# Optimization experiments

Measured on AMD Instinct MI355X. Metric: run time of the kernel, lower is better.

Reference implementation:

```python
import jax, jax.numpy as jnp
import numpy as np

B, N, D, S, ITERS, EPS = 32, 4096, 512, 8, 3, 1e-8


def layer_norm(x, g, b, eps=1e-5):
    mu = jnp.mean(x, axis=-1, keepdims=True)
    var = jnp.var(x, axis=-1, keepdims=True)
    return (x - mu) * jax.lax.rsqrt(var + eps) * g + b


def setup_inputs() -> dict:
    key = jax.random.key(0)
    ks = jax.random.split(key, 12)
    sc = 1.0 / np.sqrt(D)
    return {
        "inputs": jax.random.normal(ks[0], (B, N, D), jnp.float32),
        "noise": jax.random.normal(ks[1], (B, S, D), jnp.float32),
        "slots_mu": jax.random.normal(ks[2], (1, S, D), jnp.float32),
        "slots_sigma": jnp.ones((1, S, D), jnp.float32),
        "ln_in_g": jnp.ones((D,), jnp.float32), "ln_in_b": jnp.zeros((D,), jnp.float32),
        "ln_s_g": jnp.ones((D,), jnp.float32), "ln_s_b": jnp.zeros((D,), jnp.float32),
        "wq": jax.random.normal(ks[3], (D, D), jnp.float32) * sc,
        "wk": jax.random.normal(ks[4], (D, D), jnp.float32) * sc,
        "wv": jax.random.normal(ks[5], (D, D), jnp.float32) * sc,
        "w_ih": jax.random.normal(ks[6], (3 * D, D), jnp.float32) * sc,
        "w_hh": jax.random.normal(ks[7], (3 * D, D), jnp.float32) * sc,
        "b_ih": jnp.zeros((3 * D,), jnp.float32),
        "b_hh": jnp.zeros((3 * D,), jnp.float32),
        "ln_m_g": jnp.ones((D,), jnp.float32), "ln_m_b": jnp.zeros((D,), jnp.float32),
        "w1": jax.random.normal(ks[8], (D, D), jnp.float32) * sc,
        "b1": jnp.zeros((D,), jnp.float32),
        "w2": jax.random.normal(ks[9], (D, D), jnp.float32) * sc,
        "b2": jnp.zeros((D,), jnp.float32),
    }


def reference(inputs, noise, slots_mu, slots_sigma, ln_in_g, ln_in_b, ln_s_g, ln_s_b,
              wq, wk, wv, w_ih, w_hh, b_ih, b_hh, ln_m_g, ln_m_b, w1, b1, w2, b2):
    # slot init: mu + sigma * N(0,1)
    slots = slots_mu + slots_sigma * noise          # (B,S,D)
    x = layer_norm(inputs, ln_in_g, ln_in_b)        # (B,N,D)
    k = jnp.einsum('bnd,ed->bne', x, wk)            # (B,N,D)
    v = jnp.einsum('bnd,ed->bne', x, wv)            # (B,N,D)
    for _ in range(ITERS):
        slots_prev = slots
        sn = layer_norm(slots, ln_s_g, ln_s_b)
        q = jnp.einsum('bsd,ed->bse', sn, wq)       # (B,S,D)
        logits = jnp.einsum('bnd,bsd->bns', k, q)   # (B,N,S)
        attn = jax.nn.softmax(logits, axis=-1) + EPS  # softmax over slots
        attn = attn / jnp.sum(attn, axis=-1, keepdims=True)
        attn_t = jnp.swapaxes(attn, -1, -2)         # (B,S,N)
        updates = jnp.einsum('bsn,bnd->bsd', attn_t, v)
        # GRUCell(input=updates, hidden=slots_prev)
        gi = jnp.einsum('bsd,ed->bse', updates, w_ih) + b_ih
        gh = jnp.einsum('bsd,ed->bse', slots_prev, w_hh) + b_hh
        gi_r, gi_z, gi_n = jnp.split(gi, 3, axis=-1)
        gh_r, gh_z, gh_n = jnp.split(gh, 3, axis=-1)
        r = jax.nn.sigmoid(gi_r + gh_r)
        z = jax.nn.sigmoid(gi_z + gh_z)
        n = jnp.tanh(gi_n + r * gh_n)
        slots = (1.0 - z) * n + z * slots_prev
        # residual MLP
        h = layer_norm(slots, ln_m_g, ln_m_b)
        h = jax.nn.relu(jnp.einsum('bsd,ed->bse', h, w1) + b1)
        slots = slots + jnp.einsum('bsd,ed->bse', h, w2) + b2
    return slots
```

## Files before the change

### kernel.cpp

```cpp
#include <hip/hip_runtime.h>

#define B_ 32
#define N_ 4096
#define D_ 512
#define S_ 8
#define ITERS_ 3

__device__ __forceinline__ float sigmoid_f(float x) {
    return 1.0f / (1.0f + __expf(-x));
}
__device__ __forceinline__ float tanh_f(float x) {
    float e = __expf(2.0f * x);
    return 1.0f - 2.0f / (e + 1.0f);
}

template<int WT, int LNA>
__device__ void gemm_body(const float* __restrict__ A, const float* __restrict__ W,
                          const float* __restrict__ bias, float* __restrict__ C,
                          int M, int N, int K, int bxi, int byi,
                          const float* __restrict__ stats,
                          const float* __restrict__ lng, const float* __restrict__ lnb,
                          float* smem) {
    float (*As)[68] = (float (*)[68])smem;
    float (*Ws)[36] = (float (*)[36])(smem + 64 * 68);
    int t  = threadIdx.x;
    int bm = byi * 64, bn = bxi * 32;
    int tm = t >> 4, tn = t & 15;
    float acc[4][2] = {{0.f,0.f},{0.f,0.f},{0.f,0.f},{0.f,0.f}};

    for (int kk = 0; kk < K; kk += 64) {
        __syncthreads();
        if (WT == 2) {
#pragma unroll
            for (int r = 0; r < 4; ++r) {
                int idx = t + r * 256;
                int k = idx >> 4, m4 = idx & 15;
                float4 a4 = *(const float4*)(A + (size_t)(kk + k) * M + bm + (m4 << 2));
                *(float4*)&As[k][m4 << 2] = a4;
            }
        } else {
#pragma unroll
            for (int r = 0; r < 4; ++r) {
                int flat = t * 4 + r * 1024;
                int m = flat >> 6, k = flat & 63;
                float4 a4 = *(const float4*)(A + (size_t)(bm + m) * K + kk + k);
                if (LNA) {
                    float mean = stats[(bm + m) * 2];
                    float rs   = stats[(bm + m) * 2 + 1];
                    float4 g4 = *(const float4*)(lng + kk + k);
                    float4 b4 = *(const float4*)(lnb + kk + k);
                    a4.x = fmaf((a4.x - mean) * rs, g4.x, b4.x);
                    a4.y = fmaf((a4.y - mean) * rs, g4.y, b4.y);
                    a4.z = fmaf((a4.z - mean) * rs, g4.z, b4.z);
                    a4.w = fmaf((a4.w - mean) * rs, g4.w, b4.w);
                }
                As[k + 0][m] = a4.x; As[k + 1][m] = a4.y;
                As[k + 2][m] = a4.z; As[k + 3][m] = a4.w;
            }
        }
        if (WT == 1) {
#pragma unroll
            for (int r = 0; r < 2; ++r) {
                int flat = t * 4 + r * 1024;
                int n = flat >> 6, k = flat & 63;
                float4 w4 = *(const float4*)(W + (size_t)(bn + n) * K + kk + k);
                Ws[k + 0][n] = w4.x; Ws[k + 1][n] = w4.y;
                Ws[k + 2][n] = w4.z; Ws[k + 3][n] = w4.w;
            }
        } else {
#pragma unroll
            for (int r = 0; r < 2; ++r) {
                int flat = t * 4 + r * 1024;
                int k = flat >> 5, n = flat & 31;
                float4 w4 = *(const float4*)(W + (size_t)(kk + k) * N + bn + n);
                *(float4*)&Ws[k][n] = w4;
            }
        }
        __syncthreads();
#pragma unroll
        for (int k = 0; k < 64; ++k) {
            float4 a = *(const float4*)&As[k][tm << 2];
            float2 w = *(const float2*)&Ws[k][tn << 1];
            acc[0][0] = fmaf(a.x, w.x, acc[0][0]); acc[0][1] = fmaf(a.x, w.y, acc[0][1]);
            acc[1][0] = fmaf(a.y, w.x, acc[1][0]); acc[1][1] = fmaf(a.y, w.y, acc[1][1]);
            acc[2][0] = fmaf(a.z, w.x, acc[2][0]); acc[2][1] = fmaf(a.z, w.y, acc[2][1]);
            acc[3][0] = fmaf(a.w, w.x, acc[3][0]); acc[3][1] = fmaf(a.w, w.y, acc[3][1]);
        }
    }
#pragma unroll
    for (int i = 0; i < 4; ++i) {
#pragma unroll
        for (int j = 0; j < 2; ++j) {
            int row = bm + (tm << 2) + i;
            int col = bn + (tn << 1) + j;
            float v = acc[i][j];
            if (bias) v += bias[col];
            C[(size_t)row * N + col] = v;
        }
    }
}

__device__ void init_body(const float* __restrict__ noise, const float* __restrict__ mu,
                          const float* __restrict__ sg, float* __restrict__ slots,
                          float* __restrict__ stats, int blk) {
    int wid = threadIdx.x >> 6, lane = threadIdx.x & 63;
    int row = blk * 4 + wid;
    const float4* nz = (const float4*)(noise + (size_t)row * D_);
    const float4* m4 = (const float4*)(mu + (size_t)(row & 7) * D_);
    const float4* s4 = (const float4*)(sg + (size_t)(row & 7) * D_);
    float4 v0 = nz[lane], v1 = nz[64 + lane];
    float4 a0 = m4[lane], a1 = m4[64 + lane];
    float4 c0 = s4[lane], c1 = s4[64 + lane];
    v0.x = fmaf(c0.x, v0.x, a0.x); v0.y = fmaf(c0.y, v0.y, a0.y);
    v0.z = fmaf(c0.z, v0.z, a0.z); v0.w = fmaf(c0.w, v0.w, a0.w);
    v1.x = fmaf(c1.x, v1.x, a1.x); v1.y = fmaf(c1.y, v1.y, a1.y);
    v1.z = fmaf(c1.z, v1.z, a1.z); v1.w = fmaf(c1.w, v1.w, a1.w);
    float4* o4 = (float4*)(slots + (size_t)row * D_);
    o4[lane] = v0; o4[64 + lane] = v1;
    float s1 = v0.x + v0.y + v0.z + v0.w + v1.x + v1.y + v1.z + v1.w;
    float s2 = v0.x*v0.x; s2 = fmaf(v0.y,v0.y,s2); s2 = fmaf(v0.z,v0.z,s2); s2 = fmaf(v0.w,v0.w,s2);
    s2 = fmaf(v1.x,v1.x,s2); s2 = fmaf(v1.y,v1.y,s2); s2 = fmaf(v1.z,v1.z,s2); s2 = fmaf(v1.w,v1.w,s2);
#pragma unroll
    for (int off = 32; off > 0; off >>= 1) {
        s1 += __shfl_xor(s1, off, 64);
        s2 += __shfl_xor(s2, off, 64);
    }
    if (lane == 0) {
        float mean = s1 * (1.0f / D_);
        float var  = s2 * (1.0f / D_) - mean * mean;
        stats[row * 2]     = mean;
        stats[row * 2 + 1] = rsqrtf(var + 1e-5f);
    }
}

__global__ __launch_bounds__(256) void k_pro(const float* __restrict__ wk, const float* __restrict__ wq,
                                             const float* __restrict__ w_ih, const float* __restrict__ wv,
                                             float* __restrict__ Mqk, float* __restrict__ Wiv,
                                             const float* __restrict__ noise, const float* __restrict__ mu,
                                             const float* __restrict__ sg, float* __restrict__ slots,
                                             float* __restrict__ stats) {
    __shared__ float smem[64 * 68 + 64 * 36];
    int blk = blockIdx.x;
    if (blk < 128) {
        gemm_body<2,0>(wk, wq, nullptr, Mqk, 512, 512, 512, blk & 15, blk >> 4,
                       nullptr, nullptr, nullptr, smem);
    } else if (blk < 512) {
        int t2 = blk - 128;
        gemm_body<0,0>(w_ih, wv, nullptr, Wiv, 1536, 512, 512, t2 & 15, t2 >> 4,
                       nullptr, nullptr, nullptr, smem);
    } else {
        init_body(noise, mu, sg, slots, stats, blk - 512);
    }
}

template<int WT, int LNA>
__global__ __launch_bounds__(256) void k_gemm(const float* __restrict__ A, const float* __restrict__ W,
                                              const float* __restrict__ bias, float* __restrict__ C,
                                              int M, int N, int K,
                                              const float* __restrict__ stats,
                                              const float* __restrict__ lng, const float* __restrict__ lnb) {
    __shared__ float smem[64 * 68 + 64 * 36];
    gemm_body<WT,LNA>(A, W, bias, C, M, N, K, blockIdx.x, blockIdx.y, stats, lng, lnb, smem);
}

template<int FIRST>
__global__ __launch_bounds__(512, 1) void k_attn_gh(const float* __restrict__ x,
                                                    const float* __restrict__ qk,
                                                    const float* __restrict__ g,
                                                    const float* __restrict__ bvec,
                                                    float* __restrict__ part,
                                                    float* __restrict__ bsum,
                                                    float2* __restrict__ murs,
                                                    const float* __restrict__ slots,
                                                    const float* __restrict__ w_hh,
                                                    const float* __restrict__ b_hh,
                                                    float* __restrict__ gg) {
    __shared__ float smem[8704];
    const int blk = blockIdx.x;
    const int t = threadIdx.x;

    if (blk < 96) {
        const int ci = blk % 24, ri = blk / 24;
        const int bm = ri * 64, bn = ci * 64;
        float (*As)[68] = (float (*)[68])smem;
        float (*Ws)[68] = (float (*)[68])(smem + 64 * 68);
        const int tm = t >> 5, tn = t & 31;
        float acc[4][2] = {{0.f,0.f},{0.f,0.f},{0.f,0.f},{0.f,0.f}};
        for (int kk = 0; kk < 512; kk += 64) {
            __syncthreads();
#pragma unroll
            for (int r = 0; r < 2; ++r) {
                int flat = t * 4 + r * 2048;
                int m = flat >> 6, k = flat & 63;
                float4 a4 = *(const float4*)(slots + (size_t)(bm + m) * 512 + kk + k);
                As[k + 0][m] = a4.x; As[k + 1][m] = a4.y;
                As[k + 2][m] = a4.z; As[k + 3][m] = a4.w;
            }
#pragma unroll
            for (int r = 0; r < 2; ++r) {
                int flat = t * 4 + r * 2048;
                int n = flat >> 6, k = flat & 63;
                float4 w4 = *(const float4*)(w_hh + (size_t)(bn + n) * 512 + kk + k);
                Ws[k + 0][n] = w4.x; Ws[k + 1][n] = w4.y;
                Ws[k + 2][n] = w4.z; Ws[k + 3][n] = w4.w;
            }
            __syncthreads();
#pragma unroll
            for (int k = 0; k < 64; ++k) {
                const float4 a = *(const float4*)&As[k][tm << 2];
                const float2 w = *(const float2*)&Ws[k][tn << 1];
                acc[0][0] = fmaf(a.x, w.x, acc[0][0]); acc[0][1] = fmaf(a.x, w.y, acc[0][1]);
                acc[1][0] = fmaf(a.y, w.x, acc[1][0]); acc[1][1] = fmaf(a.y, w.y, acc[1][1]);
                acc[2][0] = fmaf(a.z, w.x, acc[2][0]); acc[2][1] = fmaf(a.z, w.y, acc[2][1]);
                acc[3][0] = fmaf(a.w, w.x, acc[3][0]); acc[3][1] = fmaf(a.w, w.y, acc[3][1]);
            }
        }
#pragma unroll
        for (int i = 0; i < 4; ++i) {
#pragma unroll
            for (int j = 0; j < 2; ++j) {
                int row = bm + (tm << 2) + i;
                int col = bn + (tn << 1) + j;
                gg[(size_t)row * 3072 + col] = acc[i][j] + b_hh[col];
            }
        }
        return;
    }

    float* qts  = smem;
    float* dds  = smem + 4096;
    float* wls  = smem + 4480;
    float* mur  = smem + 4864;
    float* redA = smem + 5888;
    float* redB = smem + 5952;
    float* c12  = smem + 6016;
    float* u0s  = smem;
    const int ablk = blk - 96;
    const int nc = ablk & 7, b = ablk >> 3;
    const int w = t >> 6, lane = t & 63;
    const size_t rowbase = (size_t)b * N_ + (size_t)nc * 512;

    {
        const float4* qk4 = (const float4*)(qk + (size_t)b * 4096);
        const float4* g4 = (const float4*)g;
        const float4* b4 = (const float4*)bvec;
        float c1p[2], c2p[2];
#pragma unroll
        for (int r = 0; r < 2; ++r) {
            int f = t + r * 512;
            int k4 = f & 127, sidx = f >> 7;
            float4 v = qk4[f];
            float4 gg4 = g4[k4];
            float4 bb = b4[k4];
            float4 qv = make_float4(v.x*gg4.x, v.y*gg4.y, v.z*gg4.z, v.w*gg4.w);
            *(float4*)&qts[(k4 * 8 + (sidx ^ (k4 & 7))) * 4] = qv;
            c1p[r] = qv.x + qv.y + qv.z + qv.w;
            c2p[r] = bb.x*v.x + bb.y*v.y + bb.z*v.z + bb.w*v.w;
        }
#pragma unroll
        for (int off = 32; off > 0; off >>= 1) {
#pragma unroll
            for (int r = 0; r < 2; ++r) {
                c1p[r] += __shfl_xor(c1p[r], off, 64);
                c2p[r] += __shfl_xor(c2p[r], off, 64);
            }
        }
        if (lane == 0) {
            redA[w * 2 + 0] = c1p[0]; redA[w * 2 + 1] = c1p[1];
            redB[w * 2 + 0] = c2p[0]; redB[w * 2 + 1] = c2p[1];
        }
    }
    if (!FIRST) {
        float2 mm = murs[rowbase + t];
        mur[2 * t] = mm.x; mur[2 * t + 1] = mm.y;
    }
    __syncthreads();
    if (t < 8) {
        int s = t;
        float v1, v2;
        if (s < 4) { v1 = redA[4*s]       + redA[4*s + 2];     v2 = redB[4*s]       + redB[4*s + 2]; }
        else       { v1 = redA[4*(s-4)+1] + redA[4*(s-4)+3];   v2 = redB[4*(s-4)+1] + redB[4*(s-4)+3]; }
        c12[s] = v1; c12[8 + s] = v2;
    }
    __syncthreads();

    float4 qa[8], qb[8];
#pragma unroll
    for (int s = 0; s < 8; ++s) {
        qa[s] = *(const float4*)&qts[(lane * 8 + (s ^ (lane & 7))) * 4];
        qb[s] = *(const float4*)&qts[((64 + lane) * 8 + (s ^ (lane & 7))) * 4];
    }

    const bool hb5 = (lane & 32) != 0, hb4 = (lane & 16) != 0, hb3 = (lane & 8) != 0;
    const float cnorm = 1.0f / (1.0f + 8.0f * 1e-8f);
    const float eadd  = 1e-8f * cnorm;

    float4 acc0[8], acc1[8];
#pragma unroll
    for (int s = 0; s < 8; ++s) {
        acc0[s] = make_float4(0.f, 0.f, 0.f, 0.f);
        acc1[s] = make_float4(0.f, 0.f, 0.f, 0.f);
    }
    float aS8[8] = {0,0,0,0,0,0,0,0}, tS8[8] = {0,0,0,0,0,0,0,0};

    const float4* xg = (const float4*)(x + rowbase * D_);
    float4 cur[8], nxt[8];
    {
        int r0 = w * 4;
#pragma unroll
        for (int i = 0; i < 4; ++i) {
            cur[2*i]   = xg[(size_t)(r0 + i) * 128 + lane];
            cur[2*i+1] = xg[(size_t)(r0 + i) * 128 + 64 + lane];
        }
    }

    for (int jb = 0; jb < 16; ++jb) {
        {
            int jn = (jb < 15) ? jb + 1 : 15;
            int r0 = jn * 32 + w * 4;
#pragma unroll
            for (int i = 0; i < 4; ++i) {
                nxt[2*i]   = xg[(size_t)(r0 + i) * 128 + lane];
                nxt[2*i+1] = xg[(size_t)(r0 + i) * 128 + 64 + lane];
            }
        }
#pragma unroll
        for (int i = 0; i < 4; ++i) {
            float4 xa = cur[2*i], xb = cur[2*i+1];
            float dd[8];
#pragma unroll
            for (int s = 0; s < 8; ++s) {
                float td = xa.x * qa[s].x;
                td = fmaf(xa.y, qa[s].y, td); td = fmaf(xa.z, qa[s].z, td); td = fmaf(xa.w, qa[s].w, td);
                td = fmaf(xb.x, qb[s].x, td); td = fmaf(xb.y, qb[s].y, td);
                td = fmaf(xb.z, qb[s].z, td); td = fmaf(xb.w, qb[s].w, td);
                dd[s] = td;
            }
            float r4[4];
#pragma unroll
            for (int s = 0; s < 4; ++s) {
                float snd = hb5 ? dd[s] : dd[s + 4];
                float kp  = hb5 ? dd[s + 4] : dd[s];
                r4[s] = kp + __shfl_xor(snd, 32, 64);
            }
            float r2v[2];
#pragma unroll
            for (int s = 0; s < 2; ++s) {
                float snd = hb4 ? r4[s] : r4[s + 2];
                float kp  = hb4 ? r4[s + 2] : r4[s];
                r2v[s] = kp + __shfl_xor(snd, 16, 64);
            }
            float v;
            {
                float snd = hb3 ? r2v[0] : r2v[1];
                float kp  = hb3 ? r2v[1] : r2v[0];
                v = kp + __shfl_xor(snd, 8, 64);
            }
            v += __shfl_xor(v, 4, 64);
            v += __shfl_xor(v, 2, 64);
            v += __shfl_xor(v, 1, 64);
            int rb = w * 4 + i;
            if ((lane & 7) == 0) dds[rb * 12 + (lane >> 3)] = v;

            if (FIRST) {
                float sx = xa.x + xa.y + xa.z + xa.w + xb.x + xb.y + xb.z + xb.w;
                float sxx = xa.x*xa.x; sxx = fmaf(xa.y,xa.y,sxx); sxx = fmaf(xa.z,xa.z,sxx); sxx = fmaf(xa.w,xa.w,sxx);
                sxx = fmaf(xb.x,xb.x,sxx); sxx = fmaf(xb.y,xb.y,sxx); sxx = fmaf(xb.z,xb.z,sxx); sxx = fmaf(xb.w,xb.w,sxx);
#pragma unroll
                for (int off = 32; off > 0; off >>= 1) {
                    sx  += __shfl_xor(sx, off, 64);
                    sxx += __shfl_xor(sxx, off, 64);
                }
                float mean = sx * (1.0f / D_);
                float rs   = rsqrtf(sxx * (1.0f / D_) - mean * mean + 1e-5f);
                if (lane == 0) {
                    int br = jb * 32 + rb;
                    mur[br * 2] = mean; mur[br * 2 + 1] = rs;
                    murs[rowbase + br] = make_float2(mean, rs);
                }
            }
        }
        if (lane < 4) {
            int rb = w * 4 + lane;
            int br = jb * 32 + rb;
            float4 d03 = *(const float4*)&dds[rb * 12];
            float4 d47 = *(const float4*)&dds[rb * 12 + 4];
            float mean = mur[br * 2], rs = mur[br * 2 + 1];
            float mc = -rs * mean;
            float lg[8];
            lg[0] = fmaf(rs, d03.x, fmaf(mc, c12[0], c12[8]));
            lg[1] = fmaf(rs, d03.y, fmaf(mc, c12[1], c12[9]));
            lg[2] = fmaf(rs, d03.z, fmaf(mc, c12[2], c12[10]));
            lg[3] = fmaf(rs, d03.w, fmaf(mc, c12[3], c12[11]));
            lg[4] = fmaf(rs, d47.x, fmaf(mc, c12[4], c12[12]));
            lg[5] = fmaf(rs, d47.y, fmaf(mc, c12[5], c12[13]));
            lg[6] = fmaf(rs, d47.z, fmaf(mc, c12[6], c12[14]));
            lg[7] = fmaf(rs, d47.w, fmaf(mc, c12[7], c12[15]));
            float mx = lg[0];
#pragma unroll
            for (int s = 1; s < 8; ++s) mx = fmaxf(mx, lg[s]);
            float p[8], psum = 0.f;
#pragma unroll
            for (int s = 0; s < 8; ++s) { p[s] = __expf(lg[s] - mx); psum += p[s]; }
            float ip = cnorm / psum;
            float wv[8];
#pragma unroll
            for (int s = 0; s < 8; ++s) {
                float a = fmaf(p[s], ip, eadd);
                wv[s] = a * rs;
                aS8[s] += a;
                tS8[s] = fmaf(wv[s], mean, tS8[s]);
            }
            *(float4*)&wls[rb * 12]     = make_float4(wv[0], wv[1], wv[2], wv[3]);
            *(float4*)&wls[rb * 12 + 4] = make_float4(wv[4], wv[5], wv[6], wv[7]);
        }
#pragma unroll
        for (int i = 0; i < 4; ++i) {
            int rb = w * 4 + i;
            float4 w03 = *(const float4*)&wls[rb * 12];
            float4 w47 = *(const float4*)&wls[rb * 12 + 4];
            float4 xa = cur[2*i], xb = cur[2*i+1];
            acc0[0].x = fmaf(w03.x, xa.x, acc0[0].x); acc0[0].y = fmaf(w03.x, xa.y, acc0[0].y);
            acc0[0].z = fmaf(w03.x, xa.z, acc0[0].z); acc0[0].w = fmaf(w03.x, xa.w, acc0[0].w);
            acc1[0].x = fmaf(w03.x, xb.x, acc1[0].x); acc1[0].y = fmaf(w03.x, xb.y, acc1[0].y);
            acc1[0].z = fmaf(w03.x, xb.z, acc1[0].z); acc1[0].w = fmaf(w03.x, xb.w, acc1[0].w);
            acc0[1].x = fmaf(w03.y, xa.x, acc0[1].x); acc0[1].y = fmaf(w03.y, xa.y, acc0[1].y);
            acc0[1].z = fmaf(w03.y, xa.z, acc0[1].z); acc0[1].w = fmaf(w03.y, xa.w, acc0[1].w);
            acc1[1].x = fmaf(w03.y, xb.x, acc1[1].x); acc1[1].y = fmaf(w03.y, xb.y, acc1[1].y);
            acc1[1].z = fmaf(w03.y, xb.z, acc1[1].z); acc1[1].w = fmaf(w03.y, xb.w, acc1[1].w);
            acc0[2].x = fmaf(w03.z, xa.x, acc0[2].x); acc0[2].y = fmaf(w03.z, xa.y, acc0[2].y);
            acc0[2].z = fmaf(w03.z, xa.z, acc0[2].z); acc0[2].w = fmaf(w03.z, xa.w, acc0[2].w);
            acc1[2].x = fmaf(w03.z, xb.x, acc1[2].x); acc1[2].y = fmaf(w03.z, xb.y, acc1[2].y);
            acc1[2].z = fmaf(w03.z, xb.z, acc1[2].z); acc1[2].w = fmaf(w03.z, xb.w, acc1[2].w);
            acc0[3].x = fmaf(w03.w, xa.x, acc0[3].x); acc0[3].y = fmaf(w03.w, xa.y, acc0[3].y);
            acc0[3].z = fmaf(w03.w, xa.z, acc0[3].z); acc0[3].w = fmaf(w03.w, xa.w, acc0[3].w);
            acc1[3].x = fmaf(w03.w, xb.x, acc1[3].x); acc1[3].y = fmaf(w03.w, xb.y, acc1[3].y);
            acc1[3].z = fmaf(w03.w, xb.z, acc1[3].z); acc1[3].w = fmaf(w03.w, xb.w, acc1[3].w);
            acc0[4].x = fmaf(w47.x, xa.x, acc0[4].x); acc0[4].y = fmaf(w47.x, xa.y, acc0[4].y);
            acc0[4].z = fmaf(w47.x, xa.z, acc0[4].z); acc0[4].w = fmaf(w47.x, xa.w, acc0[4].w);
            acc1[4].x = fmaf(w47.x, xb.x, acc1[4].x); acc1[4].y = fmaf(w47.x, xb.y, acc1[4].y);
            acc1[4].z = fmaf(w47.x, xb.z, acc1[4].z); acc1[4].w = fmaf(w47.x, xb.w, acc1[4].w);
            acc0[5].x = fmaf(w47.y, xa.x, acc0[5].x); acc0[5].y = fmaf(w47.y, xa.y, acc0[5].y);
            acc0[5].z = fmaf(w47.y, xa.z, acc0[5].z); acc0[5].w = fmaf(w47.y, xa.w, acc0[5].w);
            acc1[5].x = fmaf(w47.y, xb.x, acc1[5].x); acc1[5].y = fmaf(w47.y, xb.y, acc1[5].y);
            acc1[5].z = fmaf(w47.y, xb.z, acc1[5].z); acc1[5].w = fmaf(w47.y, xb.w, acc1[5].w);
            acc0[6].x = fmaf(w47.z, xa.x, acc0[6].x); acc0[6].y = fmaf(w47.z, xa.y, acc0[6].y);
            acc0[6].z = fmaf(w47.z, xa.z, acc0[6].z); acc0[6].w = fmaf(w47.z, xa.w, acc0[6].w);
            acc1[6].x = fmaf(w47.z, xb.x, acc1[6].x); acc1[6].y = fmaf(w47.z, xb.y, acc1[6].y);
            acc1[6].z = fmaf(w47.z, xb.z, acc1[6].z); acc1[6].w = fmaf(w47.z, xb.w, acc1[6].w);
            acc0[7].x = fmaf(w47.w, xa.x, acc0[7].x); acc0[7].y = fmaf(w47.w, xa.y, acc0[7].y);
            acc0[7].z = fmaf(w47.w, xa.z, acc0[7].z); acc0[7].w = fmaf(w47.w, xa.w, acc0[7].w);
            acc1[7].x = fmaf(w47.w, xb.x, acc1[7].x); acc1[7].y = fmaf(w47.w, xb.y, acc1[7].y);
            acc1[7].z = fmaf(w47.w, xb.z, acc1[7].z); acc1[7].w = fmaf(w47.w, xb.w, acc1[7].w);
        }
#pragma unroll
        for (int i = 0; i < 8; ++i) cur[i] = nxt[i];
    }

#pragma unroll
    for (int s = 0; s < 8; ++s) {
        aS8[s] += __shfl_xor(aS8[s], 1, 64);
        aS8[s] += __shfl_xor(aS8[s], 2, 64);
        tS8[s] += __shfl_xor(tS8[s], 1, 64);
        tS8[s] += __shfl_xor(tS8[s], 2, 64);
    }
    if (lane == 0) {
#pragma unroll
        for (int s = 0; s < 8; ++s) { redA[w * 8 + s] = aS8[s]; redB[w * 8 + s] = tS8[s]; }
    }
    for (int w2 = 0; w2 < 8; ++w2) {
        if (w == w2) {
#pragma unroll
            for (int s = 0; s < 8; ++s) {
                float* p0 = &u0s[s * 512 + (lane << 2)];
                float* p1 = p0 + 256;
                if (w2 == 0) {
                    *(float4*)p0 = acc0[s];
                    *(float4*)p1 = acc1[s];
                } else {
                    float4 v0 = *(float4*)p0;
                    v0.x += acc0[s].x; v0.y += acc0[s].y; v0.z += acc0[s].z; v0.w += acc0[s].w;
                    *(float4*)p0 = v0;
                    float4 v1 = *(float4*)p1;
                    v1.x += acc1[s].x; v1.y += acc1[s].y; v1.z += acc1[s].z; v1.w += acc1[s].w;
                    *(float4*)p1 = v1;
                }
            }
        }
        __syncthreads();
    }
    if (t < 16) {
        int s = t & 7;
        const float* src = (t < 8) ? redA : redB;
        float v = 0.f;
#pragma unroll
        for (int w2 = 0; w2 < 8; ++w2) v += src[w2 * 8 + s];
        bsum[(size_t)(b * 8 + nc) * 16 + t] = v;
    }
    float4* d4 = (float4*)(part + (size_t)(b * 8 + nc) * 4096);
    const float4* s4 = (const float4*)u0s;
    d4[t] = s4[t];
    d4[t + 512] = s4[t + 512];
}

__global__ __launch_bounds__(512) void k_ured(const float* __restrict__ part,
                                              const float* __restrict__ bsum,
                                              const float* __restrict__ g,
                                              const float* __restrict__ bvec,
                                              float* __restrict__ u0) {
    const int bs = blockIdx.x;
    const int b = bs >> 3, s = bs & 7;
    const int d = threadIdx.x;
    float Av = 0.f, Tv = 0.f;
#pragma unroll
    for (int nc = 0; nc < 8; ++nc) {
        Av += bsum[(size_t)(b * 8 + nc) * 16 + s];
        Tv += bsum[(size_t)(b * 8 + nc) * 16 + 8 + s];
    }
    float p = 0.f;
#pragma unroll
    for (int nc = 0; nc < 8; ++nc)
        p += part[(size_t)(b * 8 + nc) * 4096 + s * 512 + d];
    u0[(size_t)bs * 512 + d] = fmaf(g[d], p - Tv, Av * bvec[d]);
}

__global__ __launch_bounds__(256) void k_gi(const float* __restrict__ u0,
                                            const float* __restrict__ Wiv,
                                            const float* __restrict__ b_ih,
                                            float* __restrict__ gg) {
    __shared__ float As[64][68];
    __shared__ float Ws[64][36];
    const int t = threadIdx.x;
    const int bn = blockIdx.x * 32;
    const int bm = blockIdx.y * 64;
    int tm = t >> 4, tn = t & 15;
    float acc[4][2] = {{0.f,0.f},{0.f,0.f},{0.f,0.f},{0.f,0.f}};

    for (int kk = 0; kk < 512; kk += 64) {
        __syncthreads();
#pragma unroll
        for (int r = 0; r < 4; ++r) {
            int flat = t * 4 + r * 1024;
            int m = flat >> 6, k = flat & 63;
            float4 a4 = *(const float4*)(u0 + (size_t)(bm + m) * 512 + kk + k);
            As[k + 0][m] = a4.x; As[k + 1][m] = a4.y;
            As[k + 2][m] = a4.z; As[k + 3][m] = a4.w;
        }
#pragma unroll
        for (int r = 0; r < 2; ++r) {
            int flat = t * 4 + r * 1024;
            int n = flat >> 6, k = flat & 63;
            float4 w4 = *(const float4*)(Wiv + (size_t)(bn + n) * 512 + kk + k);
            Ws[k + 0][n] = w4.x; Ws[k + 1][n] = w4.y;
            Ws[k + 2][n] = w4.z; Ws[k + 3][n] = w4.w;
        }
        __syncthreads();
#pragma unroll
        for (int k = 0; k < 64; ++k) {
            float4 a = *(const float4*)&As[k][tm << 2];
            float2 w = *(const float2*)&Ws[k][tn << 1];
            acc[0][0] = fmaf(a.x, w.x, acc[0][0]); acc[0][1] = fmaf(a.x, w.y, acc[0][1]);
            acc[1][0] = fmaf(a.y, w.x, acc[1][0]); acc[1][1] = fmaf(a.y, w.y, acc[1][1]);
            acc[2][0] = fmaf(a.z, w.x, acc[2][0]); acc[2][1] = fmaf(a.z, w.y, acc[2][1]);
            acc[3][0] = fmaf(a.w, w.x, acc[3][0]); acc[3][1] = fmaf(a.w, w.y, acc[3][1]);
        }
    }
#pragma unroll
    for (int i = 0; i < 4; ++i) {
#pragma unroll
        for (int j = 0; j < 2; ++j) {
            int row = bm + (tm << 2) + i;
            int cw  = bn + (tn << 1) + j;
            gg[(size_t)row * 3072 + 1536 + cw] = acc[i][j] + b_ih[cw];
        }
    }
}

__global__ __launch_bounds__(512) void k_p2(const float* __restrict__ gg,
                                            const float* __restrict__ slots,
                                            const float* __restrict__ w1, const float* __restrict__ b1,
                                            const float* __restrict__ w2, const float* __restrict__ b2,
                                            const float* __restrict__ wqkT,
                                            const float* __restrict__ ln_m_g, const float* __restrict__ ln_m_b,
                                            const float* __restrict__ ln_s_g, const float* __restrict__ ln_s_b,
                                            float* __restrict__ dst, float* __restrict__ qkout, int last) {
    __shared__ float s2s[2][512];
    __shared__ float t0s[2][512];
    __shared__ float hs[2][512];
    __shared__ float stat[4];
    const int t = threadIdx.x;
    const int wid = t >> 6, lane = t & 63;
    const int r0 = blockIdx.x * 2;

#pragma unroll
    for (int j = 0; j < 2; ++j) {
        int flat = t + j * 512;
        int r = flat >> 9, d = flat & 511;
        size_t row = r0 + r;
        const float* ghb = gg + row * 3072;
        const float* gib = ghb + 1536;
        float gir = gib[d], giz = gib[d + 512], gin = gib[d + 1024];
        float ghr = ghb[d], ghz = ghb[d + 512], ghn = ghb[d + 1024];
        float rr = sigmoid_f(gir + ghr);
        float zz = sigmoid_f(giz + ghz);
        float nn = tanh_f(fmaf(rr, ghn, gin));
        float sp = slots[row * 512 + d];
        s2s[r][d] = fmaf(1.0f - zz, nn, zz * sp);
    }
    __syncthreads();
    if (wid < 2) {
        const float4* sr = (const float4*)s2s[wid];
        float4 a = sr[lane], bq = sr[64 + lane];
        float s1 = a.x + a.y + a.z + a.w + bq.x + bq.y + bq.z + bq.w;
        float s2 = a.x*a.x; s2 = fmaf(a.y,a.y,s2); s2 = fmaf(a.z,a.z,s2); s2 = fmaf(a.w,a.w,s2);
        s2 = fmaf(bq.x,bq.x,s2); s2 = fmaf(bq.y,bq.y,s2); s2 = fmaf(bq.z,bq.z,s2); s2 = fmaf(bq.w,bq.w,s2);
#pragma unroll
        for (int off = 32; off > 0; off >>= 1) {
            s1 += __shfl_xor(s1, off, 64);
            s2 += __shfl_xor(s2, off, 64);
        }
        if (lane == 0) {
            float mean = s1 * (1.0f / D_);
            float var  = s2 * (1.0f / D_) - mean * mean;
            stat[wid * 2] = mean;
            stat[wid * 2 + 1] = rsqrtf(var + 1e-5f);
        }
    }
    __syncthreads();
#pragma unroll
    for (int j = 0; j < 2; ++j) {
        int flat = t + j * 512;
        int r = flat >> 9, d = flat & 511;
        t0s[r][d] = fmaf((s2s[r][d] - stat[r * 2]) * stat[r * 2 + 1], ln_m_g[d], ln_m_b[d]);
    }
    __syncthreads();
    {
        const int c = t;
        const float4* wr = (const float4*)(w1 + (size_t)c * 512);
        float a0 = 0.f, a1 = 0.f;
#pragma unroll 8
        for (int k4 = 0; k4 < 128; ++k4) {
            float4 w4 = wr[k4];
            float4 q0 = *(const float4*)&t0s[0][k4 << 2];
            float4 q1 = *(const float4*)&t0s[1][k4 << 2];
            a0 = fmaf(q0.x, w4.x, a0); a0 = fmaf(q0.y, w4.y, a0);
            a0 = fmaf(q0.z, w4.z, a0); a0 = fmaf(q0.w, w4.w, a0);
            a1 = fmaf(q1.x, w4.x, a1); a1 = fmaf(q1.y, w4.y, a1);
            a1 = fmaf(q1.z, w4.z, a1); a1 = fmaf(q1.w, w4.w, a1);
        }
        float bc = b1[c];
        hs[0][c] = fmaxf(a0 + bc, 0.f);
        hs[1][c] = fmaxf(a1 + bc, 0.f);
    }
    __syncthreads();
    {
        const int c = t;
        const float4* wr = (const float4*)(w2 + (size_t)c * 512);
        float a0 = 0.f, a1 = 0.f;
#pragma unroll 8
        for (int k4 = 0; k4 < 128; ++k4) {
            float4 w4 = wr[k4];
            float4 q0 = *(const float4*)&hs[0][k4 << 2];
            float4 q1 = *(const float4*)&hs[1][k4 << 2];
            a0 = fmaf(q0.x, w4.x, a0); a0 = fmaf(q0.y, w4.y, a0);
            a0 = fmaf(q0.z, w4.z, a0); a0 = fmaf(q0.w, w4.w, a0);
            a1 = fmaf(q1.x, w4.x, a1); a1 = fmaf(q1.y, w4.y, a1);
            a1 = fmaf(q1.z, w4.z, a1); a1 = fmaf(q1.w, w4.w, a1);
        }
        float bc = b2[c];
        float o0 = s2s[0][c] + a0 + bc;
        float o1 = s2s[1][c] + a1 + bc;
        dst[(size_t)r0 * 512 + c] = o0;
        dst[(size_t)(r0 + 1) * 512 + c] = o1;
        s2s[0][c] = o0;
        s2s[1][c] = o1;
    }
    if (last) return;
    __syncthreads();
    if (wid < 2) {
        const float4* sr = (const float4*)s2s[wid];
        float4 a = sr[lane], bq = sr[64 + lane];
        float s1 = a.x + a.y + a.z + a.w + bq.x + bq.y + bq.z + bq.w;
        float s2 = a.x*a.x; s2 = fmaf(a.y,a.y,s2); s2 = fmaf(a.z,a.z,s2); s2 = fmaf(a.w,a.w,s2);
        s2 = fmaf(bq.x,bq.x,s2); s2 = fmaf(bq.y,bq.y,s2); s2 = fmaf(bq.z,bq.z,s2); s2 = fmaf(bq.w,bq.w,s2);
#pragma unroll
        for (int off = 32; off > 0; off >>= 1) {
            s1 += __shfl_xor(s1, off, 64);
            s2 += __shfl_xor(s2, off, 64);
        }
        if (lane == 0) {
            float mean = s1 * (1.0f / D_);
            float var  = s2 * (1.0f / D_) - mean * mean;
            stat[wid * 2] = mean;
            stat[wid * 2 + 1] = rsqrtf(var + 1e-5f);
        }
    }
    __syncthreads();
#pragma unroll
    for (int j = 0; j < 2; ++j) {
        int flat = t + j * 512;
        int r = flat >> 9, d = flat & 511;
        t0s[r][d] = fmaf((s2s[r][d] - stat[r * 2]) * stat[r * 2 + 1], ln_s_g[d], ln_s_b[d]);
    }
    __syncthreads();
    {
        const int c = t;
        const float4* wr = (const float4*)(wqkT + (size_t)c * 512);
        float a0 = 0.f, a1 = 0.f;
#pragma unroll 8
        for (int k4 = 0; k4 < 128; ++k4) {
            float4 w4 = wr[k4];
            float4 q0 = *(const float4*)&t0s[0][k4 << 2];
            float4 q1 = *(const float4*)&t0s[1][k4 << 2];
            a0 = fmaf(q0.x, w4.x, a0); a0 = fmaf(q0.y, w4.y, a0);
            a0 = fmaf(q0.z, w4.z, a0); a0 = fmaf(q0.w, w4.w, a0);
            a1 = fmaf(q1.x, w4.x, a1); a1 = fmaf(q1.y, w4.y, a1);
            a1 = fmaf(q1.z, w4.z, a1); a1 = fmaf(q1.w, w4.w, a1);
        }
        qkout[(size_t)r0 * 512 + c] = a0;
        qkout[(size_t)(r0 + 1) * 512 + c] = a1;
    }
}

extern "C" void kernel_launch(void* const* d_in, const int* in_sizes, int n_in,
                              void* d_out, int out_size, void* d_ws, size_t ws_size,
                              hipStream_t stream) {
    const float* inputs  = (const float*)d_in[0];
    const float* noise   = (const float*)d_in[1];
    const float* mu      = (const float*)d_in[2];
    const float* sg      = (const float*)d_in[3];
    const float* ln_in_g = (const float*)d_in[4];
    const float* ln_in_b = (const float*)d_in[5];
    const float* ln_s_g  = (const float*)d_in[6];
    const float* ln_s_b  = (const float*)d_in[7];
    const float* wq      = (const float*)d_in[8];
    const float* wk      = (const float*)d_in[9];
    const float* wv      = (const float*)d_in[10];
    const float* w_ih    = (const float*)d_in[11];
    const float* w_hh    = (const float*)d_in[12];
    const float* b_ih    = (const float*)d_in[13];
    const float* b_hh    = (const float*)d_in[14];
    const float* ln_m_g  = (const float*)d_in[15];
    const float* ln_m_b  = (const float*)d_in[16];
    const float* w1      = (const float*)d_in[17];
    const float* b1      = (const float*)d_in[18];
    const float* w2      = (const float*)d_in[19];
    const float* b2      = (const float*)d_in[20];

    float* ws = (float*)d_ws;
    const size_t SLOT = (size_t)B_ * S_ * D_;
    size_t o = 0;
    float* slots = ws + o; o += SLOT;
    float* qk    = ws + o; o += SLOT;
    float* u0    = ws + o; o += SLOT;
    float* gg    = ws + o; o += (size_t)256 * 3072;
    float* Mqk   = ws + o; o += (size_t)D_ * D_;
    float* Wiv   = ws + o; o += (size_t)3 * D_ * D_;
    float* statsS= ws + o; o += 512;
    float* part  = ws + o; o += (size_t)8 * B_ * 4096;
    float* bsum  = ws + o; o += (size_t)B_ * 8 * 16;
    float2* murs = (float2*)(ws + o); o += (size_t)2 * B_ * N_;

    k_pro<<<576, 256, 0, stream>>>(wk, wq, w_ih, wv, Mqk, Wiv, noise, mu, sg, slots, statsS);
    k_gemm<1,1><<<dim3(16, 4), 256, 0, stream>>>(slots, Mqk, nullptr, qk,
                                                 256, 512, 512, statsS, ln_s_g, ln_s_b);

    for (int it = 0; it < ITERS_; ++it) {
        if (it == 0)
            k_attn_gh<1><<<352, 512, 0, stream>>>(inputs, qk, ln_in_g, ln_in_b, part, bsum,
                                                  murs, slots, w_hh, b_hh, gg);
        else
            k_attn_gh<0><<<352, 512, 0, stream>>>(inputs, qk, ln_in_g, ln_in_b, part, bsum,
                                                  murs, slots, w_hh, b_hh, gg);
        k_ured<<<256, 512, 0, stream>>>(part, bsum, ln_in_g, ln_in_b, u0);
        k_gi<<<dim3(48, 4), 256, 0, stream>>>(u0, Wiv, b_ih, gg);
        int last = (it == ITERS_ - 1);
        float* dst = last ? (float*)d_out : slots;
        k_p2<<<128, 512, 0, stream>>>(gg, slots, w1, b1, w2, b2, Mqk,
                                      ln_m_g, ln_m_b, ln_s_g, ln_s_b, dst, qk, last);
    }
}
```

Measured before the change: 664.6 us.

## Fold GRU hidden GEMM into attention blocks and use one row per block in p2

```diff
diff --git a/kernel.cpp b/kernel.cpp
--- a/kernel.cpp
+++ b/kernel.cpp
@@ -224,7 +224,7 @@
                 gg[(size_t)row * 3072 + col] = acc[i][j] + b_hh[col];
             }
         }
-        return;
+        __syncthreads();
     }
 
     float* qts  = smem;
@@ -235,8 +235,7 @@
     float* redB = smem + 5952;
     float* c12  = smem + 6016;
     float* u0s  = smem;
-    const int ablk = blk - 96;
-    const int nc = ablk & 7, b = ablk >> 3;
+    const int nc = blk & 7, b = blk >> 3;
     const int w = t >> 6, lane = t & 63;
     const size_t rowbase = (size_t)b * N_ + (size_t)nc * 512;
 
@@ -584,141 +583,109 @@
                                             const float* __restrict__ ln_m_g, const float* __restrict__ ln_m_b,
                                             const float* __restrict__ ln_s_g, const float* __restrict__ ln_s_b,
                                             float* __restrict__ dst, float* __restrict__ qkout, int last) {
-    __shared__ float s2s[2][512];
-    __shared__ float t0s[2][512];
-    __shared__ float hs[2][512];
-    __shared__ float stat[4];
+    __shared__ float s2[512];
+    __shared__ float t0[512];
+    __shared__ float hh[512];
+    __shared__ float red[16];
+    __shared__ float stat[2];
     const int t = threadIdx.x;
-    const int wid = t >> 6, lane = t & 63;
-    const int r0 = blockIdx.x * 2;
-
-#pragma unroll
-    for (int j = 0; j < 2; ++j) {
-        int flat = t + j * 512;
-        int r = flat >> 9, d = flat & 511;
-        size_t row = r0 + r;
+    const int w = t >> 6, lane = t & 63;
+    const size_t row = blockIdx.x;
+
+    float s2v;
+    {
         const float* ghb = gg + row * 3072;
         const float* gib = ghb + 1536;
-        float gir = gib[d], giz = gib[d + 512], gin = gib[d + 1024];
-        float ghr = ghb[d], ghz = ghb[d + 512], ghn = ghb[d + 1024];
+        float gir = gib[t], giz = gib[t + 512], gin = gib[t + 1024];
+        float ghr = ghb[t], ghz = ghb[t + 512], ghn = ghb[t + 1024];
         float rr = sigmoid_f(gir + ghr);
         float zz = sigmoid_f(giz + ghz);
         float nn = tanh_f(fmaf(rr, ghn, gin));
-        float sp = slots[row * 512 + d];
-        s2s[r][d] = fmaf(1.0f - zz, nn, zz * sp);
-    }
-    __syncthreads();
-    if (wid < 2) {
-        const float4* sr = (const float4*)s2s[wid];
-        float4 a = sr[lane], bq = sr[64 + lane];
-        float s1 = a.x + a.y + a.z + a.w + bq.x + bq.y + bq.z + bq.w;
-        float s2 = a.x*a.x; s2 = fmaf(a.y,a.y,s2); s2 = fmaf(a.z,a.z,s2); s2 = fmaf(a.w,a.w,s2);
-        s2 = fmaf(bq.x,bq.x,s2); s2 = fmaf(bq.y,bq.y,s2); s2 = fmaf(bq.z,bq.z,s2); s2 = fmaf(bq.w,bq.w,s2);
+        float sp = slots[row * 512 + t];
+        s2v = fmaf(1.0f - zz, nn, zz * sp);
+        s2[t] = s2v;
+    }
+    {
+        float s1 = s2v, sq = s2v * s2v;
 #pragma unroll
         for (int off = 32; off > 0; off >>= 1) {
             s1 += __shfl_xor(s1, off, 64);
-            s2 += __shfl_xor(s2, off, 64);
-        }
-        if (lane == 0) {
-            float mean = s1 * (1.0f / D_);
-            float var  = s2 * (1.0f / D_) - mean * mean;
-            stat[wid * 2] = mean;
-            stat[wid * 2 + 1] = rsqrtf(var + 1e-5f);
-        }
-    }
-    __syncthreads();
-#pragma unroll
-    for (int j = 0; j < 2; ++j) {
-        int flat = t + j * 512;
-        int r = flat >> 9, d = flat & 511;
-        t0s[r][d] = fmaf((s2s[r][d] - stat[r * 2]) * stat[r * 2 + 1], ln_m_g[d], ln_m_b[d]);
-    }
+            sq += __shfl_xor(sq, off, 64);
+        }
+        if (lane == 0) { red[w] = s1; red[8 + w] = sq; }
+        __syncthreads();
+        if (t == 0) {
+            float t1 = 0.f, t2 = 0.f;
+#pragma unroll
+            for (int i = 0; i < 8; ++i) { t1 += red[i]; t2 += red[8 + i]; }
+            float mean = t1 * (1.0f / D_);
+            stat[0] = mean;
+            stat[1] = rsqrtf(t2 * (1.0f / D_) - mean * mean + 1e-5f);
+        }
+        __syncthreads();
+    }
+    t0[t] = fmaf((s2v - stat[0]) * stat[1], ln_m_g[t], ln_m_b[t]);
     __syncthreads();
     {
-        const int c = t;
-        const float4* wr = (const float4*)(w1 + (size_t)c * 512);
-        float a0 = 0.f, a1 = 0.f;
+        const float4* wr = (const float4*)(w1 + (size_t)t * 512);
+        float a = 0.f;
 #pragma unroll 8
         for (int k4 = 0; k4 < 128; ++k4) {
             float4 w4 = wr[k4];
-            float4 q0 = *(const float4*)&t0s[0][k4 << 2];
-            float4 q1 = *(const float4*)&t0s[1][k4 << 2];
-            a0 = fmaf(q0.x, w4.x, a0); a0 = fmaf(q0.y, w4.y, a0);
-            a0 = fmaf(q0.z, w4.z, a0); a0 = fmaf(q0.w, w4.w, a0);
-            a1 = fmaf(q1.x, w4.x, a1); a1 = fmaf(q1.y, w4.y, a1);
-            a1 = fmaf(q1.z, w4.z, a1); a1 = fmaf(q1.w, w4.w, a1);
-        }
-        float bc = b1[c];
-        hs[0][c] = fmaxf(a0 + bc, 0.f);
-        hs[1][c] = fmaxf(a1 + bc, 0.f);
+            float4 q0 = *(const float4*)&t0[k4 << 2];
+            a = fmaf(q0.x, w4.x, a); a = fmaf(q0.y, w4.y, a);
+            a = fmaf(q0.z, w4.z, a); a = fmaf(q0.w, w4.w, a);
+        }
+        hh[t] = fmaxf(a + b1[t], 0.f);
     }
     __syncthreads();
+    float ov;
     {
-        const int c = t;
-        const float4* wr = (const float4*)(w2 + (size_t)c * 512);
-        float a0 = 0.f, a1 = 0.f;
+        const float4* wr = (const float4*)(w2 + (size_t)t * 512);
+        float a = 0.f;
 #pragma unroll 8
         for (int k4 = 0; k4 < 128; ++k4) {
             float4 w4 = wr[k4];
-            float4 q0 = *(const float4*)&hs[0][k4 << 2];
-            float4 q1 = *(const float4*)&hs[1][k4 << 2];
-            a0 = fmaf(q0.x, w4.x, a0); a0 = fmaf(q0.y, w4.y, a0);
-            a0 = fmaf(q0.z, w4.z, a0); a0 = fmaf(q0.w, w4.w, a0);
-            a1 = fmaf(q1.x, w4.x, a1); a1 = fmaf(q1.y, w4.y, a1);
-            a1 = fmaf(q1.z, w4.z, a1); a1 = fmaf(q1.w, w4.w, a1);
-        }
-        float bc = b2[c];
-        float o0 = s2s[0][c] + a0 + bc;
-        float o1 = s2s[1][c] + a1 + bc;
-        dst[(size_t)r0 * 512 + c] = o0;
-        dst[(size_t)(r0 + 1) * 512 + c] = o1;
-        s2s[0][c] = o0;
-        s2s[1][c] = o1;
+            float4 q0 = *(const float4*)&hh[k4 << 2];
+            a = fmaf(q0.x, w4.x, a); a = fmaf(q0.y, w4.y, a);
+            a = fmaf(q0.z, w4.z, a); a = fmaf(q0.w, w4.w, a);
+        }
+        ov = s2[t] + a + b2[t];
+        dst[row * 512 + t] = ov;
     }
     if (last) return;
-    __syncthreads();
-    if (wid < 2) {
-        const float4* sr = (const float4*)s2s[wid];
-        float4 a = sr[lane], bq = sr[64 + lane];
-        float s1 = a.x + a.y + a.z + a.w + bq.x + bq.y + bq.z + bq.w;
-        float s2 = a.x*a.x; s2 = fmaf(a.y,a.y,s2); s2 = fmaf(a.z,a.z,s2); s2 = fmaf(a.w,a.w,s2);
-        s2 = fmaf(bq.x,bq.x,s2); s2 = fmaf(bq.y,bq.y,s2); s2 = fmaf(bq.z,bq.z,s2); s2 = fmaf(bq.w,bq.w,s2);
+    {
+        float s1 = ov, sq = ov * ov;
 #pragma unroll
         for (int off = 32; off > 0; off >>= 1) {
             s1 += __shfl_xor(s1, off, 64);
-            s2 += __shfl_xor(s2, off, 64);
-        }
-        if (lane == 0) {
-            float mean = s1 * (1.0f / D_);
-            float var  = s2 * (1.0f / D_) - mean * mean;
-            stat[wid * 2] = mean;
-            stat[wid * 2 + 1] = rsqrtf(var + 1e-5f);
-        }
-    }
-    __syncthreads();
-#pragma unroll
-    for (int j = 0; j < 2; ++j) {
-        int flat = t + j * 512;
-        int r = flat >> 9, d = flat & 511;
-        t0s[r][d] = fmaf((s2s[r][d] - stat[r * 2]) * stat[r * 2 + 1], ln_s_g[d], ln_s_b[d]);
-    }
+            sq += __shfl_xor(sq, off, 64);
+        }
+        if (lane == 0) { red[w] = s1; red[8 + w] = sq; }
+        __syncthreads();
+        if (t == 0) {
+            float t1 = 0.f, t2 = 0.f;
+#pragma unroll
+            for (int i = 0; i < 8; ++i) { t1 += red[i]; t2 += red[8 + i]; }
+            float mean = t1 * (1.0f / D_);
+            stat[0] = mean;
+            stat[1] = rsqrtf(t2 * (1.0f / D_) - mean * mean + 1e-5f);
+        }
+        __syncthreads();
+    }
+    t0[t] = fmaf((ov - stat[0]) * stat[1], ln_s_g[t], ln_s_b[t]);
     __syncthreads();
     {
-        const int c = t;
-        const float4* wr = (const float4*)(wqkT + (size_t)c * 512);
-        float a0 = 0.f, a1 = 0.f;
+        const float4* wr = (const float4*)(wqkT + (size_t)t * 512);
+        float a = 0.f;
 #pragma unroll 8
         for (int k4 = 0; k4 < 128; ++k4) {
             float4 w4 = wr[k4];
-            float4 q0 = *(const float4*)&t0s[0][k4 << 2];
-            float4 q1 = *(const float4*)&t0s[1][k4 << 2];
-            a0 = fmaf(q0.x, w4.x, a0); a0 = fmaf(q0.y, w4.y, a0);
-            a0 = fmaf(q0.z, w4.z, a0); a0 = fmaf(q0.w, w4.w, a0);
-            a1 = fmaf(q1.x, w4.x, a1); a1 = fmaf(q1.y, w4.y, a1);
-            a1 = fmaf(q1.z, w4.z, a1); a1 = fmaf(q1.w, w4.w, a1);
-        }
-        qkout[(size_t)r0 * 512 + c] = a0;
-        qkout[(size_t)(r0 + 1) * 512 + c] = a1;
+            float4 q0 = *(const float4*)&t0[k4 << 2];
+            a = fmaf(q0.x, w4.x, a); a = fmaf(q0.y, w4.y, a);
+            a = fmaf(q0.z, w4.z, a); a = fmaf(q0.w, w4.w, a);
+        }
+        qkout[row * 512 + t] = a;
     }
 }
 
@@ -767,16 +734,16 @@
 
     for (int it = 0; it < ITERS_; ++it) {
         if (it == 0)
-            k_attn_gh<1><<<352, 512, 0, stream>>>(inputs, qk, ln_in_g, ln_in_b, part, bsum,
+            k_attn_gh<1><<<256, 512, 0, stream>>>(inputs, qk, ln_in_g, ln_in_b, part, bsum,
                                                   murs, slots, w_hh, b_hh, gg);
         else
-            k_attn_gh<0><<<352, 512, 0, stream>>>(inputs, qk, ln_in_g, ln_in_b, part, bsum,
+            k_attn_gh<0><<<256, 512, 0, stream>>>(inputs, qk, ln_in_g, ln_in_b, part, bsum,
                                                   murs, slots, w_hh, b_hh, gg);
         k_ured<<<256, 512, 0, stream>>>(part, bsum, ln_in_g, ln_in_b, u0);
         k_gi<<<dim3(48, 4), 256, 0, stream>>>(u0, Wiv, b_ih, gg);
         int last = (it == ITERS_ - 1);
         float* dst = last ? (float*)d_out : slots;
-        k_p2<<<128, 512, 0, stream>>>(gg, slots, w1, b1, w2, b2, Mqk,
+        k_p2<<<256, 512, 0, stream>>>(gg, slots, w1, b1, w2, b2, Mqk,
                                       ln_m_g, ln_m_b, ln_s_g, ln_s_b, dst, qk, last);
     }
 }
```

New measurement: 661.9 us. About the same (-0.4%).
